# Kernel tuning notes

Hardware: AMD Instinct MI355X
Metric: run time of the kernel (lower is better)

The kernel has to match this reference:

```python
import jax, jax.numpy as jnp
import numpy as np


def setup_inputs() -> dict:
    key = jax.random.key(0)
    k1, k2, k3 = jax.random.split(key, 3)
    B, H, HKV, S, D = 2, 32, 8, 2048, 128
    q = jax.random.normal(k1, (B, H, S, D), dtype=jnp.float32)
    k = jax.random.normal(k2, (B, HKV, S, D), dtype=jnp.float32)
    v = jax.random.normal(k3, (B, HKV, S, D), dtype=jnp.float32)
    return {"q": q, "k": k, "v": v}


def reference(q, k, v):
    # GQA: query head j attends with KV head j // num_groups (repeat_interleave
    # semantics). Instead of materializing repeated K/V, reshape Q into
    # [B, Hkv, G, S, D] and contract against shared KV heads directly.
    B, H, S, D = q.shape
    Hkv = k.shape[1]
    G = H // Hkv
    qg = q.reshape(B, Hkv, G, S, D)
    scale = 1.0 / jnp.sqrt(jnp.asarray(D, q.dtype))
    # scores: [B, Hkv, G, Sq, Sk]
    scores = jnp.einsum('bhgqd,bhkd->bhgqk', qg, k) * scale
    # is_causal=True: lower-triangular mask
    causal = jnp.tril(jnp.ones((S, S), dtype=bool))
    scores = jnp.where(causal, scores, jnp.finfo(scores.dtype).min)
    attn = jax.nn.softmax(scores, axis=-1)
    out = jnp.einsum('bhgqk,bhkd->bhgqd', attn, v)
    return out.reshape(B, H, S, D)
```

## Files before the change

### kernel.cpp

```cpp
#include <hip/hip_runtime.h>
#include <hip/hip_bf16.h>
#include <cstdint>

typedef __bf16 bf16;
typedef __bf16 bf16x8 __attribute__((ext_vector_type(8)));
typedef float f32x4 __attribute__((ext_vector_type(4)));
typedef unsigned int u32;
typedef __attribute__((address_space(3))) uint32_t lds_u32;
typedef const __attribute__((address_space(1))) uint32_t glb_u32;

#define B_ 2
#define H_ 32
#define HKV_ 8
#define S_ 2048
#define D_ 128
#define QT 128
#define KT 128
#define NQT (S_ / QT)
#define NIMG (S_ / 64)
#define IMG_ELEMS (64 * D_)
#define NEG_BIG (-1.0e30f)
#define SCL 0.12751745f
#define DEFER_THR 8.0f

__device__ __forceinline__ bf16x8 cvt8p(float4 a, float4 b) {
  bf16x8 r = {(bf16)a.x, (bf16)a.y, (bf16)a.z, (bf16)a.w,
              (bf16)b.x, (bf16)b.y, (bf16)b.z, (bf16)b.w};
  return r;
}
__device__ __forceinline__ bf16x8 cvt8(const float* f) {
  return cvt8p(*(const float4*)f, *(const float4*)(f + 4));
}
__device__ __forceinline__ bf16x8 cvt8s(const float* f, float s) {
  float4 a = *(const float4*)f, b = *(const float4*)(f + 4);
  bf16x8 r = {(bf16)(a.x * s), (bf16)(a.y * s), (bf16)(a.z * s), (bf16)(a.w * s),
              (bf16)(b.x * s), (bf16)(b.y * s), (bf16)(b.z * s), (bf16)(b.w * s)};
  return r;
}
__device__ __forceinline__ u32 pk2(float lo, float hi) {
  union { bf16 h[2]; u32 w; } u;
  u.h[0] = (bf16)lo; u.h[1] = (bf16)hi;
  return u.w;
}

__global__ __launch_bounds__(512) void prep(const float* __restrict__ k,
                                            const float* __restrict__ v,
                                            bf16* __restrict__ kws,
                                            bf16* __restrict__ vws) {
  __shared__ float Vf[64 * 129];
  const int blk = blockIdx.x;
  const int bhkv = blk >> 5, img = blk & 31;
  const float* ks = k + ((size_t)bhkv * S_ + (size_t)img * 64) * D_;
  const float* vs = v + ((size_t)bhkv * S_ + (size_t)img * 64) * D_;
  bf16* kd = kws + (size_t)blk * IMG_ELEMS;
  bf16* vd = vws + (size_t)blk * IMG_ELEMS;
  const int t = threadIdx.x;
#pragma unroll
  for (int i = 0; i < 4; ++i) {
    int c = t + 512 * i, row = c >> 5, c4 = c & 31;
    *(float4*)&Vf[row * 129 + c4 * 4] = *(const float4*)(vs + row * D_ + c4 * 4);
  }
#pragma unroll
  for (int i = 0; i < 2; ++i) {
    int chunk = t + 512 * i, row = chunk >> 4, c16 = chunk & 15;
    int e = (c16 ^ (row & 7)) << 3;
    *(bf16x8*)&kd[chunk * 8] = cvt8(ks + row * D_ + e);
  }
  __syncthreads();
#pragma unroll
  for (int i = 0; i < 2; ++i) {
    int chunk = t + 512 * i, d = chunk >> 3, c8 = chunk & 7;
    int k0 = (c8 ^ (d & 7)) << 3;
    bf16x8 val;
#pragma unroll
    for (int kk = 0; kk < 8; ++kk) val[kk] = (bf16)Vf[(k0 + kk) * 129 + d];
    *(bf16x8*)&vd[chunk * 8] = val;
  }
}

__global__ __launch_bounds__(512, 4) void fa_mfma(
    const float* __restrict__ q, const bf16* __restrict__ kws,
    const bf16* __restrict__ vws, float* __restrict__ out) {
  __shared__ bf16 Kb[2 * IMG_ELEMS];
  __shared__ bf16 Vb[2 * IMG_ELEMS];

  const int tid = threadIdx.x, wave = tid >> 6, lane = tid & 63;
  const int col = lane & 15, quad = lane >> 4;
  const int bid = blockIdx.x;
  const int tqt = (NQT - 1) - (bid >> 6);
  const int bh = bid & 63, b = bh >> 5, h = bh & 31, hkv = h >> 2;
  const int bhkv = b * HKV_ + hkv;

  const float* qh = q + (size_t)(b * H_ + h) * S_ * D_;
  float* oh = out + (size_t)(b * H_ + h) * S_ * D_;
  const bf16* kg = kws + (size_t)(bhkv * NIMG) * IMG_ELEMS;
  const bf16* vg = vws + (size_t)(bhkv * NIMG) * IMG_ELEMS;
  const int q0 = tqt * QT;
  const int jmax = tqt;

  bf16x8 qf[4];
  {
    const float* qrow = qh + (size_t)(q0 + wave * 16 + col) * D_ + quad * 8;
#pragma unroll
    for (int ks = 0; ks < 4; ++ks) qf[ks] = cvt8s(qrow + ks * 32, SCL);
  }

  f32x4 o[8];
#pragma unroll
  for (int i = 0; i < 8; ++i) o[i] = (f32x4){0.f, 0.f, 0.f, 0.f};
  float m_i = NEG_BIG, lp = 0.f;

  const int qoff = (quad * 16) ^ ((col & 7) << 4);
  const int qx[4] = {qoff, qoff ^ 64, qoff ^ 128, qoff ^ 192};

  const int stoff = tid * 16;

  auto stageK = [&](int j) {
    const char* src = (const char*)kg + (size_t)j * 32768 + stoff;
    char* dst = (char*)Kb + stoff;
#pragma unroll
    for (int i = 0; i < 4; ++i)
      __builtin_amdgcn_global_load_lds((glb_u32*)(src + i * 8192),
                                       (lds_u32*)(dst + i * 8192), 16, 0, 0);
  };
  auto stageV = [&](int j) {
    const char* src = (const char*)vg + (size_t)j * 32768 + stoff;
    char* dst = (char*)Vb + stoff;
#pragma unroll
    for (int i = 0; i < 4; ++i)
      __builtin_amdgcn_global_load_lds((glb_u32*)(src + i * 8192),
                                       (lds_u32*)(dst + i * 8192), 16, 0, 0);
  };

  stageK(0);
  stageV(0);
  asm volatile("s_waitcnt vmcnt(0)" ::: "memory");
  __builtin_amdgcn_s_barrier();
  __builtin_amdgcn_sched_barrier(0);

  for (int j = 0; j <= jmax; ++j) {
    float s[8][4];
    __builtin_amdgcn_s_setprio(1);
#pragma unroll
    for (int nt = 0; nt < 8; ++nt) {
      const char* An = (const char*)Kb + (nt * 16 + col) * 256;
      f32x4 acc = (f32x4){0.f, 0.f, 0.f, 0.f};
#pragma unroll
      for (int ks = 0; ks < 4; ++ks) {
        bf16x8 kf = *(const bf16x8*)(An + qx[ks]);
        acc = __builtin_amdgcn_mfma_f32_16x16x32_bf16(kf, qf[ks], acc, 0, 0, 0);
      }
#pragma unroll
      for (int r = 0; r < 4; ++r) s[nt][r] = acc[r];
    }
    __builtin_amdgcn_s_setprio(0);

    __builtin_amdgcn_s_barrier();
    __builtin_amdgcn_sched_barrier(0);
    if (j < jmax) stageK(j + 1);

    if (j == tqt) {
      const int rowq = wave * 16 + col;
#pragma unroll
      for (int nt = 0; nt < 8; ++nt)
#pragma unroll
        for (int r = 0; r < 4; ++r)
          if (nt * 16 + quad * 4 + r > rowq) s[nt][r] = NEG_BIG;
    }

    float m4[8];
#pragma unroll
    for (int nt = 0; nt < 8; ++nt)
      m4[nt] = fmaxf(fmaxf(s[nt][0], s[nt][1]), fmaxf(s[nt][2], s[nt][3]));
    float mx = fmaxf(fmaxf(fmaxf(m4[0], m4[1]), fmaxf(m4[2], m4[3])),
                     fmaxf(fmaxf(m4[4], m4[5]), fmaxf(m4[6], m4[7])));
    mx = fmaxf(mx, __shfl_xor(mx, 16, 64));
    mx = fmaxf(mx, __shfl_xor(mx, 32, 64));

    if (__any(mx - m_i > DEFER_THR)) {
      float mnew = fmaxf(m_i, mx);
      float alpha = exp2f(m_i - mnew);
      lp *= alpha;
      m_i = mnew;
#pragma unroll
      for (int dt = 0; dt < 8; ++dt) o[dt] *= alpha;
    }

    float rs = 0.f;
#pragma unroll
    for (int nt = 0; nt < 8; ++nt)
#pragma unroll
      for (int r = 0; r < 4; ++r) {
        s[nt][r] = exp2f(s[nt][r] - m_i);
        rs += s[nt][r];
      }
    lp += rs;

    u32 pk_[8][2];
#pragma unroll
    for (int nt = 0; nt < 8; ++nt) {
      pk_[nt][0] = pk2(s[nt][0], s[nt][1]);
      pk_[nt][1] = pk2(s[nt][2], s[nt][3]);
    }
    const bool oddq = (quad & 1);
    union W8 { u32 w[4]; bf16x8 h; } pf[4];
#pragma unroll
    for (int ks = 0; ks < 4; ++ks)
#pragma unroll
      for (int p = 0; p < 2; ++p) {
        auto sw = __builtin_amdgcn_permlane32_swap(pk_[2 * ks][p],
                                                   pk_[2 * ks + 1][p],
                                                   false, false);
        u32 Qp = (u32)sw[0], Rp = (u32)sw[1];
        u32 Tp = (u32)__shfl_xor((int)Qp, 16, 64);
        u32 Sp = (u32)__shfl_xor((int)Rp, 16, 64);
        pf[ks].w[p] = oddq ? Sp : Qp;
        pf[ks].w[2 + p] = oddq ? Rp : Tp;
      }

    if (j < jmax)
      asm volatile("s_waitcnt vmcnt(4)" ::: "memory");
    else
      asm volatile("s_waitcnt vmcnt(0)" ::: "memory");
    __builtin_amdgcn_s_barrier();
    __builtin_amdgcn_sched_barrier(0);

    __builtin_amdgcn_s_setprio(1);
#pragma unroll
    for (int dt = 0; dt < 8; ++dt) {
#pragma unroll
      for (int ks = 0; ks < 4; ++ks) {
        const char* Av = (const char*)Vb + (ks >> 1) * 16384 +
                         (dt * 16 + col) * 128 + (qoff ^ ((ks & 1) << 6));
        bf16x8 vf = *(const bf16x8*)Av;
        o[dt] = __builtin_amdgcn_mfma_f32_16x16x32_bf16(vf, pf[ks].h, o[dt], 0, 0, 0);
      }
    }
    __builtin_amdgcn_s_setprio(0);

    if (j < jmax) {
      asm volatile("s_waitcnt vmcnt(0)" ::: "memory");
      __builtin_amdgcn_s_barrier();
      __builtin_amdgcn_sched_barrier(0);
      stageV(j + 1);
    }
  }

  float l = lp;
  l += __shfl_xor(l, 16, 64);
  l += __shfl_xor(l, 32, 64);
  const float inv = 1.f / l;
  float* orow = oh + (size_t)(q0 + wave * 16 + col) * D_;
#pragma unroll
  for (int dt = 0; dt < 8; ++dt) {
    f32x4 vout = o[dt] * inv;
    *(f32x4*)&orow[dt * 16 + quad * 4] = vout;
  }
}

extern "C" void kernel_launch(void* const* d_in, const int* in_sizes, int n_in,
                              void* d_out, int out_size, void* d_ws, size_t ws_size,
                              hipStream_t stream) {
  const int QN = B_ * H_ * S_ * D_;
  int qi, ki, vi;
  if (in_sizes[0] == QN)      { qi = 0; ki = 1; vi = 2; }
  else if (in_sizes[1] == QN) { qi = 1; ki = 0; vi = 2; }
  else                        { qi = 2; ki = 0; vi = 1; }
  const float* q = (const float*)d_in[qi];
  const float* k = (const float*)d_in[ki];
  const float* v = (const float*)d_in[vi];
  float* out = (float*)d_out;

  bf16* kws = (bf16*)d_ws;
  bf16* vws = kws + (size_t)(B_ * HKV_) * NIMG * IMG_ELEMS;

  prep<<<dim3(B_ * HKV_ * NIMG), dim3(512), 0, stream>>>(k, v, kws, vws);
  fa_mfma<<<dim3(B_ * H_ * NQT), dim3(512), 0, stream>>>(q, kws, vws, out);
}
```

Before: 239.3 us.

## Halve key tile to 64 and double occupancy with balanced block order

```diff
diff --git a/kernel.cpp b/kernel.cpp
--- a/kernel.cpp
+++ b/kernel.cpp
@@ -15,7 +15,7 @@
 #define S_ 2048
 #define D_ 128
 #define QT 128
-#define KT 128
+#define KT 64
 #define NQT (S_ / QT)
 #define NIMG (S_ / 64)
 #define IMG_ELEMS (64 * D_)
@@ -78,16 +78,17 @@
   }
 }
 
-__global__ __launch_bounds__(512, 4) void fa_mfma(
+__global__ __launch_bounds__(512, 8) void fa_mfma(
     const float* __restrict__ q, const bf16* __restrict__ kws,
     const bf16* __restrict__ vws, float* __restrict__ out) {
-  __shared__ bf16 Kb[2 * IMG_ELEMS];
-  __shared__ bf16 Vb[2 * IMG_ELEMS];
+  __shared__ bf16 Kb[IMG_ELEMS];
+  __shared__ bf16 Vb[IMG_ELEMS];
 
   const int tid = threadIdx.x, wave = tid >> 6, lane = tid & 63;
   const int col = lane & 15, quad = lane >> 4;
   const int bid = blockIdx.x;
-  const int tqt = (NQT - 1) - (bid >> 6);
+  const int uu = bid >> 8, slot = (bid >> 6) & 3, tt = 4 * slot + uu;
+  const int tqt = (tt & 1) ? (tt >> 1) : (NQT - 1) - (tt >> 1);
   const int bh = bid & 63, b = bh >> 5, h = bh & 31, hkv = h >> 2;
   const int bhkv = b * HKV_ + hkv;
 
@@ -96,7 +97,7 @@
   const bf16* kg = kws + (size_t)(bhkv * NIMG) * IMG_ELEMS;
   const bf16* vg = vws + (size_t)(bhkv * NIMG) * IMG_ELEMS;
   const int q0 = tqt * QT;
-  const int jmax = tqt;
+  const int jmax = 2 * tqt + 1;
 
   bf16x8 qf[4];
   {
@@ -116,18 +117,18 @@
   const int stoff = tid * 16;
 
   auto stageK = [&](int j) {
-    const char* src = (const char*)kg + (size_t)j * 32768 + stoff;
+    const char* src = (const char*)kg + (size_t)j * 16384 + stoff;
     char* dst = (char*)Kb + stoff;
 #pragma unroll
-    for (int i = 0; i < 4; ++i)
+    for (int i = 0; i < 2; ++i)
       __builtin_amdgcn_global_load_lds((glb_u32*)(src + i * 8192),
                                        (lds_u32*)(dst + i * 8192), 16, 0, 0);
   };
   auto stageV = [&](int j) {
-    const char* src = (const char*)vg + (size_t)j * 32768 + stoff;
+    const char* src = (const char*)vg + (size_t)j * 16384 + stoff;
     char* dst = (char*)Vb + stoff;
 #pragma unroll
-    for (int i = 0; i < 4; ++i)
+    for (int i = 0; i < 2; ++i)
       __builtin_amdgcn_global_load_lds((glb_u32*)(src + i * 8192),
                                        (lds_u32*)(dst + i * 8192), 16, 0, 0);
   };
@@ -139,10 +140,10 @@
   __builtin_amdgcn_sched_barrier(0);
 
   for (int j = 0; j <= jmax; ++j) {
-    float s[8][4];
+    float s[4][4];
     __builtin_amdgcn_s_setprio(1);
 #pragma unroll
-    for (int nt = 0; nt < 8; ++nt) {
+    for (int nt = 0; nt < 4; ++nt) {
       const char* An = (const char*)Kb + (nt * 16 + col) * 256;
       f32x4 acc = (f32x4){0.f, 0.f, 0.f, 0.f};
 #pragma unroll
@@ -155,25 +156,26 @@
     }
     __builtin_amdgcn_s_setprio(0);
 
-    __builtin_amdgcn_s_barrier();
-    __builtin_amdgcn_sched_barrier(0);
-    if (j < jmax) stageK(j + 1);
-
-    if (j == tqt) {
-      const int rowq = wave * 16 + col;
-#pragma unroll
-      for (int nt = 0; nt < 8; ++nt)
+    if (j < jmax) {
+      __builtin_amdgcn_s_barrier();
+      __builtin_amdgcn_sched_barrier(0);
+      stageK(j + 1);
+    }
+
+    if (j >= 2 * tqt) {
+      const int rel = j * KT - q0 - wave * 16;
+#pragma unroll
+      for (int nt = 0; nt < 4; ++nt)
 #pragma unroll
         for (int r = 0; r < 4; ++r)
-          if (nt * 16 + quad * 4 + r > rowq) s[nt][r] = NEG_BIG;
-    }
-
-    float m4[8];
-#pragma unroll
-    for (int nt = 0; nt < 8; ++nt)
-      m4[nt] = fmaxf(fmaxf(s[nt][0], s[nt][1]), fmaxf(s[nt][2], s[nt][3]));
-    float mx = fmaxf(fmaxf(fmaxf(m4[0], m4[1]), fmaxf(m4[2], m4[3])),
-                     fmaxf(fmaxf(m4[4], m4[5]), fmaxf(m4[6], m4[7])));
+          if (rel + nt * 16 + quad * 4 + r > col) s[nt][r] = NEG_BIG;
+    }
+
+    float mx = fmaxf(fmaxf(fmaxf(s[0][0], s[0][1]), fmaxf(s[0][2], s[0][3])),
+                     fmaxf(fmaxf(s[1][0], s[1][1]), fmaxf(s[1][2], s[1][3])));
+    mx = fmaxf(mx,
+               fmaxf(fmaxf(fmaxf(s[2][0], s[2][1]), fmaxf(s[2][2], s[2][3])),
+                     fmaxf(fmaxf(s[3][0], s[3][1]), fmaxf(s[3][2], s[3][3]))));
     mx = fmaxf(mx, __shfl_xor(mx, 16, 64));
     mx = fmaxf(mx, __shfl_xor(mx, 32, 64));
 
@@ -188,7 +190,7 @@
 
     float rs = 0.f;
 #pragma unroll
-    for (int nt = 0; nt < 8; ++nt)
+    for (int nt = 0; nt < 4; ++nt)
 #pragma unroll
       for (int r = 0; r < 4; ++r) {
         s[nt][r] = exp2f(s[nt][r] - m_i);
@@ -196,16 +198,16 @@
       }
     lp += rs;
 
-    u32 pk_[8][2];
-#pragma unroll
-    for (int nt = 0; nt < 8; ++nt) {
+    u32 pk_[4][2];
+#pragma unroll
+    for (int nt = 0; nt < 4; ++nt) {
       pk_[nt][0] = pk2(s[nt][0], s[nt][1]);
       pk_[nt][1] = pk2(s[nt][2], s[nt][3]);
     }
     const bool oddq = (quad & 1);
-    union W8 { u32 w[4]; bf16x8 h; } pf[4];
-#pragma unroll
-    for (int ks = 0; ks < 4; ++ks)
+    union W8 { u32 w[4]; bf16x8 h; } pf[2];
+#pragma unroll
+    for (int ks = 0; ks < 2; ++ks)
 #pragma unroll
       for (int p = 0; p < 2; ++p) {
         auto sw = __builtin_amdgcn_permlane32_swap(pk_[2 * ks][p],
@@ -219,7 +221,7 @@
       }
 
     if (j < jmax)
-      asm volatile("s_waitcnt vmcnt(4)" ::: "memory");
+      asm volatile("s_waitcnt vmcnt(2)" ::: "memory");
     else
       asm volatile("s_waitcnt vmcnt(0)" ::: "memory");
     __builtin_amdgcn_s_barrier();
@@ -228,11 +230,10 @@
     __builtin_amdgcn_s_setprio(1);
 #pragma unroll
     for (int dt = 0; dt < 8; ++dt) {
-#pragma unroll
-      for (int ks = 0; ks < 4; ++ks) {
-        const char* Av = (const char*)Vb + (ks >> 1) * 16384 +
-                         (dt * 16 + col) * 128 + (qoff ^ ((ks & 1) << 6));
-        bf16x8 vf = *(const bf16x8*)Av;
+      const char* Av = (const char*)Vb + (dt * 16 + col) * 128;
+#pragma unroll
+      for (int ks = 0; ks < 2; ++ks) {
+        bf16x8 vf = *(const bf16x8*)(Av + qx[ks]);
         o[dt] = __builtin_amdgcn_mfma_f32_16x16x32_bf16(vf, pf[ks].h, o[dt], 0, 0, 0);
       }
     }
```

After: 576.2 us. +140.8%, slower.
